# Kernel optimization log

Hardware: AMD Instinct MI355X
Metric: run time of the kernel (lower is better)

The kernel has to match this reference:

```python
import jax, jax.numpy as jnp
import numpy as np

N_NODES = 20000
N_EDGES = 320000
N_QUERY = 100000
D = 256


def _sage_conv(x, adj_row, adj_col, Wl, bl, Wr):
    # PyG SAGEConv with mean aggregation over SparseTensor adj_t:
    #   out = lin_l(mean_{j in N(i)} x_j) + lin_r(x_i)
    # adj_row = destination node, adj_col = source node.
    n = x.shape[0]
    msg = x[adj_col]                                        # [E, D] gather
    agg = jax.ops.segment_sum(msg, adj_row, num_segments=n)  # [N, D]
    deg = jax.ops.segment_sum(jnp.ones((adj_row.shape[0],), x.dtype), adj_row,
                              num_segments=n)
    agg = agg / jnp.maximum(deg, 1.0)[:, None]               # mean reduce
    return agg @ Wl + bl + x @ Wr


def setup_inputs() -> dict:
    key = jax.random.key(0)
    ks = jax.random.split(key, 12)
    s = 1.0 / np.sqrt(D)
    return {
        "adj_row": jax.random.randint(ks[0], (N_EDGES,), 0, N_NODES, dtype=jnp.int32),
        "adj_col": jax.random.randint(ks[1], (N_EDGES,), 0, N_NODES, dtype=jnp.int32),
        "edges": jax.random.randint(ks[2], (2, N_QUERY), 0, N_NODES, dtype=jnp.int32),
        "emb": jax.random.normal(ks[3], (N_NODES, D), jnp.float32),
        "W1l": jax.random.normal(ks[4], (D, D), jnp.float32) * s,
        "b1": jnp.zeros((D,), jnp.float32),
        "W1r": jax.random.normal(ks[5], (D, D), jnp.float32) * s,
        "W2l": jax.random.normal(ks[6], (D, D), jnp.float32) * s,
        "b2": jnp.zeros((D,), jnp.float32),
        "W2r": jax.random.normal(ks[7], (D, D), jnp.float32) * s,
        "Wp1": jax.random.normal(ks[8], (D, D), jnp.float32) * s,
        "bp1": jnp.zeros((D,), jnp.float32),
        "Wp2": jax.random.normal(ks[9], (D, 1), jnp.float32) * s,
        "bp2": jnp.zeros((1,), jnp.float32),
    }


def reference(adj_row, adj_col, edges, emb, W1l, b1, W1r, W2l, b2, W2r,
              Wp1, bp1, Wp2, bp2):
    # SAGE backbone (eval mode: dropout is identity)
    x = _sage_conv(emb, adj_row, adj_col, W1l, b1, W1r)
    x = jax.nn.relu(x)
    x = _sage_conv(x, adj_row, adj_col, W2l, b2, W2r)     # [N, D]
    # LinkPredictor: h = x_i * x_j -> MLP -> sigmoid
    h = x[edges[0]] * x[edges[1]]                          # [Q, D]
    h = jax.nn.relu(h @ Wp1 + bp1)
    return jax.nn.sigmoid(h @ Wp2 + bp2)                   # [Q, 1]
```

## Files before the change

### kernel.cpp

```cpp
#include <hip/hip_runtime.h>
#include <cstddef>

constexpr int NN = 20000;
constexpr int NE = 320000;
constexpr int NQ = 100000;
constexpr int DD = 256;
constexpr int NB = (NN + 255) / 256;

typedef __attribute__((ext_vector_type(8))) short bf16x8;
typedef __attribute__((ext_vector_type(4))) float f32x4;
typedef __attribute__((ext_vector_type(4))) unsigned short u16x4;
typedef __attribute__((ext_vector_type(8))) unsigned short u16x8;

__device__ inline unsigned short f2bf(float f) {
    union { float f; unsigned u; } v; v.f = f;
    unsigned r = v.u + 0x7fffu + ((v.u >> 16) & 1u);
    return (unsigned short)(r >> 16);
}
__device__ inline float bf2f(unsigned short h) {
    union { unsigned u; float f; } t; t.u = ((unsigned)h) << 16;
    return t.f;
}

__global__ __launch_bounds__(256) void k_cast(const float* __restrict__ x,
                                              unsigned short* __restrict__ y,
                                              int* __restrict__ deg) {
    int i = blockIdx.x * 256 + threadIdx.x;
    if (i < NN) deg[i] = 0;
    if (i >= NN * DD / 8) return;
    float4 f0 = *reinterpret_cast<const float4*>(x + (size_t)i * 8);
    float4 f1 = *reinterpret_cast<const float4*>(x + (size_t)i * 8 + 4);
    u16x8 o;
    o[0] = f2bf(f0.x); o[1] = f2bf(f0.y); o[2] = f2bf(f0.z); o[3] = f2bf(f0.w);
    o[4] = f2bf(f1.x); o[5] = f2bf(f1.y); o[6] = f2bf(f1.z); o[7] = f2bf(f1.w);
    *reinterpret_cast<u16x8*>(y + (size_t)i * 8) = o;
}

__global__ __launch_bounds__(256) void k_deg(const int* __restrict__ row,
                                             int* __restrict__ deg) {
    int e = blockIdx.x * 256 + threadIdx.x;
    if (e < NE) atomicAdd(&deg[row[e]], 1);
}

__global__ __launch_bounds__(256) void k_scan1(const int* __restrict__ deg,
                                               int* __restrict__ offs,
                                               int* __restrict__ bsum) {
    __shared__ int wsum[4];
    const int tid = threadIdx.x, lane = tid & 63, wid = tid >> 6;
    int i = blockIdx.x * 256 + tid;
    int v = (i < NN) ? deg[i] : 0;
    int sc = v;
#pragma unroll
    for (int d = 1; d < 64; d <<= 1) {
        int t = __shfl_up(sc, d);
        if (lane >= d) sc += t;
    }
    if (lane == 63) wsum[wid] = sc;
    __syncthreads();
    int wpre = 0;
    for (int w = 0; w < wid; ++w) wpre += wsum[w];
    if (i < NN) offs[i] = wpre + sc - v;
    if (tid == 255) bsum[blockIdx.x] = wpre + sc;
}

__global__ __launch_bounds__(256) void k_scan2(int* __restrict__ bsum) {
    __shared__ int wsum[4];
    const int tid = threadIdx.x, lane = tid & 63, wid = tid >> 6;
    int v = (tid < NB) ? bsum[tid] : 0;
    int sc = v;
#pragma unroll
    for (int d = 1; d < 64; d <<= 1) {
        int t = __shfl_up(sc, d);
        if (lane >= d) sc += t;
    }
    if (lane == 63) wsum[wid] = sc;
    __syncthreads();
    int wpre = 0;
    for (int w = 0; w < wid; ++w) wpre += wsum[w];
    if (tid < NB) bsum[tid] = wpre + sc - v;
}

__global__ __launch_bounds__(256) void k_scan3(const int* __restrict__ deg,
                                               const int* __restrict__ bsum,
                                               int* __restrict__ offs,
                                               int* __restrict__ cursor,
                                               float* __restrict__ recip) {
    int i = blockIdx.x * 256 + threadIdx.x;
    if (i < NN) {
        int o = offs[i] + bsum[i >> 8];
        offs[i] = o;
        cursor[i] = o;
        recip[i] = 1.0f / fmaxf((float)deg[i], 1.0f);
    }
    if (i == 0) offs[NN] = NE;
}

__global__ __launch_bounds__(256) void k_fill(const int* __restrict__ row,
                                              const int* __restrict__ col,
                                              int* __restrict__ cursor,
                                              int* __restrict__ scol) {
    int e = blockIdx.x * 256 + threadIdx.x;
    if (e < NE) {
        int r = row[e];
        int p = atomicAdd(&cursor[r], 1);
        scol[p] = col[e];
    }
}

__global__ __launch_bounds__(256) void k_packs(
    const float* __restrict__ w0, const float* __restrict__ w1,
    const float* __restrict__ w2, const float* __restrict__ w3,
    const float* __restrict__ w4,
    unsigned short* __restrict__ h0, unsigned short* __restrict__ h1,
    unsigned short* __restrict__ h2, unsigned short* __restrict__ h3,
    unsigned short* __restrict__ h4,
    unsigned short* __restrict__ l0, unsigned short* __restrict__ l1,
    unsigned short* __restrict__ l2, unsigned short* __restrict__ l3) {
    int m = blockIdx.x >> 5;
    int idx = (blockIdx.x & 31) * 256 + threadIdx.x;
    const float* W = (m == 0) ? w0 : (m == 1) ? w1 : (m == 2) ? w2 : (m == 3) ? w3 : w4;
    unsigned short* H = (m == 0) ? h0 : (m == 1) ? h1 : (m == 2) ? h2 : (m == 3) ? h3 : h4;
    unsigned short* L = (m == 0) ? l0 : (m == 1) ? l1 : (m == 2) ? l2 : (m == 3) ? l3 : nullptr;
    int t = idx >> 6, lane = idx & 63;
    int kt = t >> 4, nt = t & 15;
    int k0 = kt * 32 + (lane >> 4) * 8;
    int n = nt * 16 + (lane & 15);
    unsigned uh[4], ul[4];
#pragma unroll
    for (int i = 0; i < 4; ++i) {
        float fa = W[(size_t)(k0 + 2 * i) * DD + n];
        float fb = W[(size_t)(k0 + 2 * i + 1) * DD + n];
        unsigned short ha = f2bf(fa), hb = f2bf(fb);
        unsigned short la = f2bf(fa - bf2f(ha)), lb = f2bf(fb - bf2f(hb));
        uh[i] = (unsigned)ha | ((unsigned)hb << 16);
        ul[i] = (unsigned)la | ((unsigned)lb << 16);
    }
    *reinterpret_cast<uint4*>(H + (size_t)idx * 8) = make_uint4(uh[0], uh[1], uh[2], uh[3]);
    if (L)
        *reinterpret_cast<uint4*>(L + (size_t)idx * 8) = make_uint4(ul[0], ul[1], ul[2], ul[3]);
}

__global__ __launch_bounds__(256) void k_lin(
    const unsigned short* __restrict__ A,
    const unsigned short* __restrict__ Wlh, const unsigned short* __restrict__ Wll,
    const unsigned short* __restrict__ Wrh, const unsigned short* __restrict__ Wrl,
    unsigned short* __restrict__ P, unsigned short* __restrict__ Q) {
    const int nq   = blockIdx.x & 3;
    const int mblk = blockIdx.x >> 2;
    const int wave = threadIdx.x >> 6;
    const int lane = threadIdx.x & 63;
    const int row0 = mblk * 64 + wave * 16;
    const int kcol = (lane >> 4) * 8;
    const int ar = min(row0 + (lane & 15), NN - 1);

    f32x4 accP[4], accQ[4];
#pragma unroll
    for (int nt = 0; nt < 4; ++nt) {
        accP[nt] = {0, 0, 0, 0};
        accQ[nt] = {0, 0, 0, 0};
    }

#pragma unroll 2
    for (int kt = 0; kt < 8; ++kt) {
        bf16x8 a1 = *reinterpret_cast<const bf16x8*>(A + (size_t)ar * DD + kt * 32 + kcol);
#pragma unroll
        for (int nt = 0; nt < 4; ++nt) {
            const size_t fo = ((size_t)((kt * 16 + nq * 4 + nt) * 64 + lane)) * 8;
            bf16x8 blh = *reinterpret_cast<const bf16x8*>(Wlh + fo);
            bf16x8 bll = *reinterpret_cast<const bf16x8*>(Wll + fo);
            bf16x8 brh = *reinterpret_cast<const bf16x8*>(Wrh + fo);
            bf16x8 brl = *reinterpret_cast<const bf16x8*>(Wrl + fo);
            accP[nt] = __builtin_amdgcn_mfma_f32_16x16x32_bf16(a1, blh, accP[nt], 0, 0, 0);
            accP[nt] = __builtin_amdgcn_mfma_f32_16x16x32_bf16(a1, bll, accP[nt], 0, 0, 0);
            accQ[nt] = __builtin_amdgcn_mfma_f32_16x16x32_bf16(a1, brh, accQ[nt], 0, 0, 0);
            accQ[nt] = __builtin_amdgcn_mfma_f32_16x16x32_bf16(a1, brl, accQ[nt], 0, 0, 0);
        }
    }

    const int n0 = lane & 15;
    const int rg = (lane >> 4) * 4;
#pragma unroll
    for (int nt = 0; nt < 4; ++nt) {
        int n = (nq * 4 + nt) * 16 + n0;
#pragma unroll
        for (int j = 0; j < 4; ++j) {
            int r = row0 + rg + j;
            if (r < NN) {
                P[(size_t)r * DD + n] = f2bf(accP[nt][j]);
                Q[(size_t)r * DD + n] = f2bf(accQ[nt][j]);
            }
        }
    }
}

template <int RELU>
__global__ __launch_bounds__(256) void k_gath(const int* __restrict__ offs,
                                              const int* __restrict__ scol,
                                              const float* __restrict__ recip,
                                              const unsigned short* __restrict__ P,
                                              const unsigned short* __restrict__ Q,
                                              const float* __restrict__ b,
                                              unsigned short* __restrict__ out) {
    int node = blockIdx.x * 4 + (threadIdx.x >> 6);
    int lane = threadIdx.x & 63;
    if (node >= NN) return;
    int s = offs[node];
    int e = offs[node + 1];
    const int half = lane >> 5;
    const int l32 = lane & 31;
    float acc[8] = {0, 0, 0, 0, 0, 0, 0, 0};
    float acc2[8] = {0, 0, 0, 0, 0, 0, 0, 0};
    int p = s;
    for (; p + 3 < e; p += 4) {
        int c0 = scol[p + half];
        int c1 = scol[p + 2 + half];
        u16x8 v0 = *reinterpret_cast<const u16x8*>(P + (size_t)c0 * DD + l32 * 8);
        u16x8 v1 = *reinterpret_cast<const u16x8*>(P + (size_t)c1 * DD + l32 * 8);
#pragma unroll
        for (int i = 0; i < 8; ++i) {
            acc[i] += bf2f(v0[i]);
            acc2[i] += bf2f(v1[i]);
        }
    }
    for (; p + 1 < e; p += 2) {
        int c0 = scol[p + half];
        u16x8 v0 = *reinterpret_cast<const u16x8*>(P + (size_t)c0 * DD + l32 * 8);
#pragma unroll
        for (int i = 0; i < 8; ++i) acc[i] += bf2f(v0[i]);
    }
    if (p < e && half == 0) {
        int c0 = scol[p];
        u16x8 v0 = *reinterpret_cast<const u16x8*>(P + (size_t)c0 * DD + l32 * 8);
#pragma unroll
        for (int i = 0; i < 8; ++i) acc2[i] += bf2f(v0[i]);
    }
    float rc = recip[node];
    u16x8 q = *reinterpret_cast<const u16x8*>(Q + (size_t)node * DD + l32 * 8);
    float4 b0 = *reinterpret_cast<const float4*>(b + l32 * 8);
    float4 b1 = *reinterpret_cast<const float4*>(b + l32 * 8 + 4);
    float bb[8] = {b0.x, b0.y, b0.z, b0.w, b1.x, b1.y, b1.z, b1.w};
    u16x8 o;
#pragma unroll
    for (int i = 0; i < 8; ++i) {
        float t = acc[i] + acc2[i];
        t += __shfl_xor(t, 32);
        t = t * rc + bf2f(q[i]) + bb[i];
        if (RELU) t = fmaxf(t, 0.0f);
        o[i] = f2bf(t);
    }
    if (half == 0)
        *reinterpret_cast<u16x8*>(out + (size_t)node * DD + l32 * 8) = o;
}

__global__ __launch_bounds__(512, 4) void k_pred(const int* __restrict__ edges,
                                                 const unsigned short* __restrict__ x2,
                                                 const unsigned short* __restrict__ Wp1p,
                                                 const float* __restrict__ bp1,
                                                 const float* __restrict__ Wp2,
                                                 const float* __restrict__ bp2,
                                                 float* __restrict__ out) {
    __shared__ unsigned short sh[128 * 256];
    const int tid = threadIdx.x;
    const int wave = tid >> 6;
    const int lane = tid & 63;
    const int q0 = blockIdx.x * 128;

    const int grow = tid >> 4;
    const int t16 = tid & 15;
#pragma unroll
    for (int s = 0; s < 4; ++s) {
        int r = s * 32 + grow;
        int q = q0 + r;
        u16x8 p0 = {0, 0, 0, 0, 0, 0, 0, 0};
        u16x8 p1 = {0, 0, 0, 0, 0, 0, 0, 0};
        if (q < NQ) {
            int a = edges[q];
            int c = edges[NQ + q];
            const unsigned short* pa = x2 + (size_t)a * DD + t16 * 16;
            const unsigned short* pc = x2 + (size_t)c * DD + t16 * 16;
            u16x8 ua0 = *reinterpret_cast<const u16x8*>(pa);
            u16x8 ua1 = *reinterpret_cast<const u16x8*>(pa + 8);
            u16x8 uc0 = *reinterpret_cast<const u16x8*>(pc);
            u16x8 uc1 = *reinterpret_cast<const u16x8*>(pc + 8);
#pragma unroll
            for (int i = 0; i < 8; ++i) {
                p0[i] = f2bf(bf2f(ua0[i]) * bf2f(uc0[i]));
                p1[i] = f2bf(bf2f(ua1[i]) * bf2f(uc1[i]));
            }
        }
        int swz = (r & 7) << 3;
        *reinterpret_cast<u16x8*>(&sh[r * 256 + ((t16 * 16) ^ swz)]) = p0;
        *reinterpret_cast<u16x8*>(&sh[r * 256 + ((t16 * 16 + 8) ^ swz)]) = p1;
    }
    __syncthreads();

    f32x4 acc[8][2];
#pragma unroll
    for (int m = 0; m < 8; ++m)
#pragma unroll
        for (int n = 0; n < 2; ++n) acc[m][n] = {0, 0, 0, 0};

    const int akoff = (lane >> 4) * 8;
    const int arl = lane & 15;
    for (int kt = 0; kt < 8; ++kt) {
        bf16x8 af[8];
#pragma unroll
        for (int m = 0; m < 8; ++m) {
            int row = m * 16 + arl;
            af[m] = *reinterpret_cast<const bf16x8*>(
                &sh[row * 256 + ((kt * 32 + akoff) ^ ((row & 7) << 3))]);
        }
#pragma unroll
        for (int ntl = 0; ntl < 2; ++ntl) {
            int nt = wave * 2 + ntl;
            bf16x8 bfrag = *reinterpret_cast<const bf16x8*>(
                Wp1p + ((size_t)((kt * 16 + nt) * 64 + lane)) * 8);
#pragma unroll
            for (int m = 0; m < 8; ++m)
                acc[m][ntl] = __builtin_amdgcn_mfma_f32_16x16x32_bf16(af[m], bfrag, acc[m][ntl], 0, 0, 0);
        }
    }

    float rs[8][4];
#pragma unroll
    for (int m = 0; m < 8; ++m)
#pragma unroll
        for (int j = 0; j < 4; ++j) rs[m][j] = 0.0f;
#pragma unroll
    for (int ntl = 0; ntl < 2; ++ntl) {
        int n = (wave * 2 + ntl) * 16 + (lane & 15);
        float bias = bp1[n];
        float w2 = Wp2[n];
#pragma unroll
        for (int m = 0; m < 8; ++m)
#pragma unroll
            for (int j = 0; j < 4; ++j)
                rs[m][j] += fmaxf(acc[m][ntl][j] + bias, 0.0f) * w2;
    }
#pragma unroll
    for (int msk = 1; msk < 16; msk <<= 1) {
#pragma unroll
        for (int m = 0; m < 8; ++m)
#pragma unroll
            for (int j = 0; j < 4; ++j) rs[m][j] += __shfl_xor(rs[m][j], msk);
    }

    float* psum = reinterpret_cast<float*>(sh);
    __syncthreads();
    if ((lane & 15) == 0) {
        int rg = (lane >> 4) * 4;
#pragma unroll
        for (int m = 0; m < 8; ++m)
#pragma unroll
            for (int j = 0; j < 4; ++j)
                psum[wave * 128 + m * 16 + rg + j] = rs[m][j];
    }
    __syncthreads();

    if (tid < 128) {
        int q = q0 + tid;
        if (q < NQ) {
            float z = bp2[0];
#pragma unroll
            for (int w = 0; w < 8; ++w) z += psum[w * 128 + tid];
            out[q] = 1.0f / (1.0f + expf(-z));
        }
    }
}

extern "C" void kernel_launch(void* const* d_in, const int* in_sizes, int n_in,
                              void* d_out, int out_size, void* d_ws, size_t ws_size,
                              hipStream_t stream) {
    const int*   adj_row = (const int*)d_in[0];
    const int*   adj_col = (const int*)d_in[1];
    const int*   edges   = (const int*)d_in[2];
    const float* emb     = (const float*)d_in[3];
    const float* W1l     = (const float*)d_in[4];
    const float* b1      = (const float*)d_in[5];
    const float* W1r     = (const float*)d_in[6];
    const float* W2l     = (const float*)d_in[7];
    const float* b2      = (const float*)d_in[8];
    const float* W2r     = (const float*)d_in[9];
    const float* Wp1     = (const float*)d_in[10];
    const float* bp1     = (const float*)d_in[11];
    const float* Wp2     = (const float*)d_in[12];
    const float* bp2     = (const float*)d_in[13];
    float* out = (float*)d_out;

    const size_t featH = (size_t)NN * DD * 2;
    const size_t packBytes = (size_t)DD * DD * 2;

    char* ws = (char*)d_ws;
    size_t off = 0;
    unsigned short* P  = (unsigned short*)(ws + off); off += featH;
    unsigned short* Q  = (unsigned short*)(ws + off); off += featH;
    unsigned short* x1 = (unsigned short*)(ws + off); off += featH;
    unsigned short* xh = (unsigned short*)(ws + off); off += featH;
    int*   deg    = (int*)(ws + off);   off += (size_t)NN * 4;
    int*   offs   = (int*)(ws + off);   off += (size_t)(NN + 1) * 4;
    int*   cursor = (int*)(ws + off);   off += (size_t)NN * 4;
    float* recip  = (float*)(ws + off); off += (size_t)NN * 4;
    int*   bsum   = (int*)(ws + off);   off += (size_t)NB * 4;
    int*   scol   = (int*)(ws + off);   off += (size_t)NE * 4;
    unsigned short* Wp1p = (unsigned short*)(ws + off); off += packBytes;
    unsigned short* pk[8];
    for (int i = 0; i < 8; ++i) { pk[i] = (unsigned short*)(ws + off); off += packBytes; }

    const int MB4 = ((NN + 63) / 64) * 4;

    k_cast<<<(NN * DD / 8 + 255) / 256, 256, 0, stream>>>(emb, xh, deg);
    k_deg<<<(NE + 255) / 256, 256, 0, stream>>>(adj_row, deg);
    k_scan1<<<NB, 256, 0, stream>>>(deg, offs, bsum);
    k_scan2<<<1, 256, 0, stream>>>(bsum);
    k_scan3<<<NB, 256, 0, stream>>>(deg, bsum, offs, cursor, recip);
    k_fill<<<(NE + 255) / 256, 256, 0, stream>>>(adj_row, adj_col, cursor, scol);
    k_packs<<<160, 256, 0, stream>>>(W1l, W1r, W2l, W2r, Wp1,
                                     pk[0], pk[2], pk[4], pk[6], Wp1p,
                                     pk[1], pk[3], pk[5], pk[7]);

    k_lin<<<MB4, 256, 0, stream>>>(xh, pk[0], pk[1], pk[2], pk[3], P, Q);
    k_gath<1><<<(NN + 3) / 4, 256, 0, stream>>>(offs, scol, recip, P, Q, b1, x1);

    unsigned short* x2 = xh;
    k_lin<<<MB4, 256, 0, stream>>>(x1, pk[4], pk[5], pk[6], pk[7], P, Q);
    k_gath<0><<<(NN + 3) / 4, 256, 0, stream>>>(offs, scol, recip, P, Q, b2, x2);

    k_pred<<<(NQ + 127) / 128, 512, 0, stream>>>(edges, x2, Wp1p, bp1, Wp2, bp2, out);
}
```

Before: 195.4 us.

## Merge cast and weight packing, retile linear GEMM, deepen gather unrolling

Three independent changes. First, the feature cast and the weight pack kernels are merged into one launch to remove one kernel launch. Second, the linear MFMA kernel now gives each wave 32 rows by 32 columns instead of 16 rows by 64 columns, so each B fragment load is reused across two A tiles. Third, the neighbor gather loop processes 8 edges per iteration with 4 independent accumulators to keep more loads in flight. These add register pressure and change the order of the floating-point sums.

```diff
diff --git a/kernel.cpp b/kernel.cpp
--- a/kernel.cpp
+++ b/kernel.cpp
@@ -6,6 +6,7 @@
 constexpr int NQ = 100000;
 constexpr int DD = 256;
 constexpr int NB = (NN + 255) / 256;
+constexpr int CASTB = (NN * DD / 8 + 255) / 256;
 
 typedef __attribute__((ext_vector_type(8))) short bf16x8;
 typedef __attribute__((ext_vector_type(4))) float f32x4;
@@ -22,18 +23,53 @@
     return t.f;
 }
 
-__global__ __launch_bounds__(256) void k_cast(const float* __restrict__ x,
-                                              unsigned short* __restrict__ y,
-                                              int* __restrict__ deg) {
-    int i = blockIdx.x * 256 + threadIdx.x;
-    if (i < NN) deg[i] = 0;
-    if (i >= NN * DD / 8) return;
-    float4 f0 = *reinterpret_cast<const float4*>(x + (size_t)i * 8);
-    float4 f1 = *reinterpret_cast<const float4*>(x + (size_t)i * 8 + 4);
-    u16x8 o;
-    o[0] = f2bf(f0.x); o[1] = f2bf(f0.y); o[2] = f2bf(f0.z); o[3] = f2bf(f0.w);
-    o[4] = f2bf(f1.x); o[5] = f2bf(f1.y); o[6] = f2bf(f1.z); o[7] = f2bf(f1.w);
-    *reinterpret_cast<u16x8*>(y + (size_t)i * 8) = o;
+__global__ __launch_bounds__(256) void k_castpack(
+    const float* __restrict__ x, unsigned short* __restrict__ y,
+    int* __restrict__ deg,
+    const float* __restrict__ w0, const float* __restrict__ w1,
+    const float* __restrict__ w2, const float* __restrict__ w3,
+    const float* __restrict__ w4,
+    unsigned short* __restrict__ h0, unsigned short* __restrict__ h1,
+    unsigned short* __restrict__ h2, unsigned short* __restrict__ h3,
+    unsigned short* __restrict__ h4,
+    unsigned short* __restrict__ l0, unsigned short* __restrict__ l1,
+    unsigned short* __restrict__ l2, unsigned short* __restrict__ l3) {
+    const int bid = blockIdx.x;
+    if (bid < CASTB) {
+        int i = bid * 256 + threadIdx.x;
+        if (i < NN) deg[i] = 0;
+        if (i >= NN * DD / 8) return;
+        float4 f0 = *reinterpret_cast<const float4*>(x + (size_t)i * 8);
+        float4 f1 = *reinterpret_cast<const float4*>(x + (size_t)i * 8 + 4);
+        u16x8 o;
+        o[0] = f2bf(f0.x); o[1] = f2bf(f0.y); o[2] = f2bf(f0.z); o[3] = f2bf(f0.w);
+        o[4] = f2bf(f1.x); o[5] = f2bf(f1.y); o[6] = f2bf(f1.z); o[7] = f2bf(f1.w);
+        *reinterpret_cast<u16x8*>(y + (size_t)i * 8) = o;
+        return;
+    }
+    int mb = bid - CASTB;
+    int m = mb >> 5;
+    int idx = (mb & 31) * 256 + threadIdx.x;
+    const float* W = (m == 0) ? w0 : (m == 1) ? w1 : (m == 2) ? w2 : (m == 3) ? w3 : w4;
+    unsigned short* H = (m == 0) ? h0 : (m == 1) ? h1 : (m == 2) ? h2 : (m == 3) ? h3 : h4;
+    unsigned short* L = (m == 0) ? l0 : (m == 1) ? l1 : (m == 2) ? l2 : (m == 3) ? l3 : nullptr;
+    int t = idx >> 6, lane = idx & 63;
+    int kt = t >> 4, nt = t & 15;
+    int k0 = kt * 32 + (lane >> 4) * 8;
+    int n = nt * 16 + (lane & 15);
+    unsigned uh[4], ul[4];
+#pragma unroll
+    for (int i = 0; i < 4; ++i) {
+        float fa = W[(size_t)(k0 + 2 * i) * DD + n];
+        float fb = W[(size_t)(k0 + 2 * i + 1) * DD + n];
+        unsigned short ha = f2bf(fa), hb = f2bf(fb);
+        unsigned short la = f2bf(fa - bf2f(ha)), lb = f2bf(fb - bf2f(hb));
+        uh[i] = (unsigned)ha | ((unsigned)hb << 16);
+        ul[i] = (unsigned)la | ((unsigned)lb << 16);
+    }
+    *reinterpret_cast<uint4*>(H + (size_t)idx * 8) = make_uint4(uh[0], uh[1], uh[2], uh[3]);
+    if (L)
+        *reinterpret_cast<uint4*>(L + (size_t)idx * 8) = make_uint4(ul[0], ul[1], ul[2], ul[3]);
 }
 
 __global__ __launch_bounds__(256) void k_deg(const int* __restrict__ row,
@@ -107,90 +143,67 @@
     }
 }
 
-__global__ __launch_bounds__(256) void k_packs(
-    const float* __restrict__ w0, const float* __restrict__ w1,
-    const float* __restrict__ w2, const float* __restrict__ w3,
-    const float* __restrict__ w4,
-    unsigned short* __restrict__ h0, unsigned short* __restrict__ h1,
-    unsigned short* __restrict__ h2, unsigned short* __restrict__ h3,
-    unsigned short* __restrict__ h4,
-    unsigned short* __restrict__ l0, unsigned short* __restrict__ l1,
-    unsigned short* __restrict__ l2, unsigned short* __restrict__ l3) {
-    int m = blockIdx.x >> 5;
-    int idx = (blockIdx.x & 31) * 256 + threadIdx.x;
-    const float* W = (m == 0) ? w0 : (m == 1) ? w1 : (m == 2) ? w2 : (m == 3) ? w3 : w4;
-    unsigned short* H = (m == 0) ? h0 : (m == 1) ? h1 : (m == 2) ? h2 : (m == 3) ? h3 : h4;
-    unsigned short* L = (m == 0) ? l0 : (m == 1) ? l1 : (m == 2) ? l2 : (m == 3) ? l3 : nullptr;
-    int t = idx >> 6, lane = idx & 63;
-    int kt = t >> 4, nt = t & 15;
-    int k0 = kt * 32 + (lane >> 4) * 8;
-    int n = nt * 16 + (lane & 15);
-    unsigned uh[4], ul[4];
-#pragma unroll
-    for (int i = 0; i < 4; ++i) {
-        float fa = W[(size_t)(k0 + 2 * i) * DD + n];
-        float fb = W[(size_t)(k0 + 2 * i + 1) * DD + n];
-        unsigned short ha = f2bf(fa), hb = f2bf(fb);
-        unsigned short la = f2bf(fa - bf2f(ha)), lb = f2bf(fb - bf2f(hb));
-        uh[i] = (unsigned)ha | ((unsigned)hb << 16);
-        ul[i] = (unsigned)la | ((unsigned)lb << 16);
-    }
-    *reinterpret_cast<uint4*>(H + (size_t)idx * 8) = make_uint4(uh[0], uh[1], uh[2], uh[3]);
-    if (L)
-        *reinterpret_cast<uint4*>(L + (size_t)idx * 8) = make_uint4(ul[0], ul[1], ul[2], ul[3]);
-}
-
 __global__ __launch_bounds__(256) void k_lin(
     const unsigned short* __restrict__ A,
     const unsigned short* __restrict__ Wlh, const unsigned short* __restrict__ Wll,
     const unsigned short* __restrict__ Wrh, const unsigned short* __restrict__ Wrl,
     unsigned short* __restrict__ P, unsigned short* __restrict__ Q) {
-    const int nq   = blockIdx.x & 3;
-    const int mblk = blockIdx.x >> 2;
+    const int ns   = blockIdx.x & 7;
+    const int mblk = blockIdx.x >> 3;
     const int wave = threadIdx.x >> 6;
     const int lane = threadIdx.x & 63;
-    const int row0 = mblk * 64 + wave * 16;
+    const int row0 = mblk * 128 + wave * 32;
     const int kcol = (lane >> 4) * 8;
-    const int ar = min(row0 + (lane & 15), NN - 1);
-
-    f32x4 accP[4], accQ[4];
-#pragma unroll
-    for (int nt = 0; nt < 4; ++nt) {
-        accP[nt] = {0, 0, 0, 0};
-        accQ[nt] = {0, 0, 0, 0};
-    }
+    const int ar0 = min(row0 + (lane & 15), NN - 1);
+    const int ar1 = min(row0 + 16 + (lane & 15), NN - 1);
+
+    f32x4 accP[2][2], accQ[2][2];
+#pragma unroll
+    for (int mt = 0; mt < 2; ++mt)
+#pragma unroll
+        for (int nt = 0; nt < 2; ++nt) {
+            accP[mt][nt] = {0, 0, 0, 0};
+            accQ[mt][nt] = {0, 0, 0, 0};
+        }
 
 #pragma unroll 2
     for (int kt = 0; kt < 8; ++kt) {
-        bf16x8 a1 = *reinterpret_cast<const bf16x8*>(A + (size_t)ar * DD + kt * 32 + kcol);
-#pragma unroll
-        for (int nt = 0; nt < 4; ++nt) {
-            const size_t fo = ((size_t)((kt * 16 + nq * 4 + nt) * 64 + lane)) * 8;
+        bf16x8 a0 = *reinterpret_cast<const bf16x8*>(A + (size_t)ar0 * DD + kt * 32 + kcol);
+        bf16x8 a1 = *reinterpret_cast<const bf16x8*>(A + (size_t)ar1 * DD + kt * 32 + kcol);
+#pragma unroll
+        for (int nt = 0; nt < 2; ++nt) {
+            const size_t fo = ((size_t)((kt * 16 + ns * 2 + nt) * 64 + lane)) * 8;
             bf16x8 blh = *reinterpret_cast<const bf16x8*>(Wlh + fo);
             bf16x8 bll = *reinterpret_cast<const bf16x8*>(Wll + fo);
             bf16x8 brh = *reinterpret_cast<const bf16x8*>(Wrh + fo);
             bf16x8 brl = *reinterpret_cast<const bf16x8*>(Wrl + fo);
-            accP[nt] = __builtin_amdgcn_mfma_f32_16x16x32_bf16(a1, blh, accP[nt], 0, 0, 0);
-            accP[nt] = __builtin_amdgcn_mfma_f32_16x16x32_bf16(a1, bll, accP[nt], 0, 0, 0);
-            accQ[nt] = __builtin_amdgcn_mfma_f32_16x16x32_bf16(a1, brh, accQ[nt], 0, 0, 0);
-            accQ[nt] = __builtin_amdgcn_mfma_f32_16x16x32_bf16(a1, brl, accQ[nt], 0, 0, 0);
+            accP[0][nt] = __builtin_amdgcn_mfma_f32_16x16x32_bf16(a0, blh, accP[0][nt], 0, 0, 0);
+            accP[1][nt] = __builtin_amdgcn_mfma_f32_16x16x32_bf16(a1, blh, accP[1][nt], 0, 0, 0);
+            accP[0][nt] = __builtin_amdgcn_mfma_f32_16x16x32_bf16(a0, bll, accP[0][nt], 0, 0, 0);
+            accP[1][nt] = __builtin_amdgcn_mfma_f32_16x16x32_bf16(a1, bll, accP[1][nt], 0, 0, 0);
+            accQ[0][nt] = __builtin_amdgcn_mfma_f32_16x16x32_bf16(a0, brh, accQ[0][nt], 0, 0, 0);
+            accQ[1][nt] = __builtin_amdgcn_mfma_f32_16x16x32_bf16(a1, brh, accQ[1][nt], 0, 0, 0);
+            accQ[0][nt] = __builtin_amdgcn_mfma_f32_16x16x32_bf16(a0, brl, accQ[0][nt], 0, 0, 0);
+            accQ[1][nt] = __builtin_amdgcn_mfma_f32_16x16x32_bf16(a1, brl, accQ[1][nt], 0, 0, 0);
         }
     }
 
     const int n0 = lane & 15;
     const int rg = (lane >> 4) * 4;
 #pragma unroll
-    for (int nt = 0; nt < 4; ++nt) {
-        int n = (nq * 4 + nt) * 16 + n0;
-#pragma unroll
-        for (int j = 0; j < 4; ++j) {
-            int r = row0 + rg + j;
-            if (r < NN) {
-                P[(size_t)r * DD + n] = f2bf(accP[nt][j]);
-                Q[(size_t)r * DD + n] = f2bf(accQ[nt][j]);
+    for (int mt = 0; mt < 2; ++mt)
+#pragma unroll
+        for (int nt = 0; nt < 2; ++nt) {
+            int n = (ns * 2 + nt) * 16 + n0;
+#pragma unroll
+            for (int j = 0; j < 4; ++j) {
+                int r = row0 + mt * 16 + rg + j;
+                if (r < NN) {
+                    P[(size_t)r * DD + n] = f2bf(accP[mt][nt][j]);
+                    Q[(size_t)r * DD + n] = f2bf(accQ[mt][nt][j]);
+                }
             }
         }
-    }
 }
 
 template <int RELU>
@@ -208,31 +221,33 @@
     int e = offs[node + 1];
     const int half = lane >> 5;
     const int l32 = lane & 31;
-    float acc[8] = {0, 0, 0, 0, 0, 0, 0, 0};
-    float acc2[8] = {0, 0, 0, 0, 0, 0, 0, 0};
+    float a0[8] = {0,0,0,0,0,0,0,0}, a1[8] = {0,0,0,0,0,0,0,0};
+    float a2[8] = {0,0,0,0,0,0,0,0}, a3[8] = {0,0,0,0,0,0,0,0};
     int p = s;
-    for (; p + 3 < e; p += 4) {
-        int c0 = scol[p + half];
-        int c1 = scol[p + 2 + half];
+    for (; p + 7 < e; p += 8) {
+        int base = p + 4 * half;
+        int c0 = scol[base], c1 = scol[base + 1], c2 = scol[base + 2], c3 = scol[base + 3];
         u16x8 v0 = *reinterpret_cast<const u16x8*>(P + (size_t)c0 * DD + l32 * 8);
         u16x8 v1 = *reinterpret_cast<const u16x8*>(P + (size_t)c1 * DD + l32 * 8);
+        u16x8 v2 = *reinterpret_cast<const u16x8*>(P + (size_t)c2 * DD + l32 * 8);
+        u16x8 v3 = *reinterpret_cast<const u16x8*>(P + (size_t)c3 * DD + l32 * 8);
 #pragma unroll
         for (int i = 0; i < 8; ++i) {
-            acc[i] += bf2f(v0[i]);
-            acc2[i] += bf2f(v1[i]);
+            a0[i] += bf2f(v0[i]); a1[i] += bf2f(v1[i]);
+            a2[i] += bf2f(v2[i]); a3[i] += bf2f(v3[i]);
         }
     }
     for (; p + 1 < e; p += 2) {
         int c0 = scol[p + half];
         u16x8 v0 = *reinterpret_cast<const u16x8*>(P + (size_t)c0 * DD + l32 * 8);
 #pragma unroll
-        for (int i = 0; i < 8; ++i) acc[i] += bf2f(v0[i]);
+        for (int i = 0; i < 8; ++i) a0[i] += bf2f(v0[i]);
     }
     if (p < e && half == 0) {
         int c0 = scol[p];
         u16x8 v0 = *reinterpret_cast<const u16x8*>(P + (size_t)c0 * DD + l32 * 8);
 #pragma unroll
-        for (int i = 0; i < 8; ++i) acc2[i] += bf2f(v0[i]);
+        for (int i = 0; i < 8; ++i) a1[i] += bf2f(v0[i]);
     }
     float rc = recip[node];
     u16x8 q = *reinterpret_cast<const u16x8*>(Q + (size_t)node * DD + l32 * 8);
@@ -242,7 +257,7 @@
     u16x8 o;
 #pragma unroll
     for (int i = 0; i < 8; ++i) {
-        float t = acc[i] + acc2[i];
+        float t = a0[i] + a1[i] + a2[i] + a3[i];
         t += __shfl_xor(t, 32);
         t = t * rc + bf2f(q[i]) + bb[i];
         if (RELU) t = fmaxf(t, 0.0f);
@@ -406,23 +421,23 @@
     unsigned short* pk[8];
     for (int i = 0; i < 8; ++i) { pk[i] = (unsigned short*)(ws + off); off += packBytes; }
 
-    const int MB4 = ((NN + 63) / 64) * 4;
-
-    k_cast<<<(NN * DD / 8 + 255) / 256, 256, 0, stream>>>(emb, xh, deg);
+    const int MB8 = ((NN + 127) / 128) * 8;
+
+    k_castpack<<<CASTB + 160, 256, 0, stream>>>(emb, xh, deg,
+                                                W1l, W1r, W2l, W2r, Wp1,
+                                                pk[0], pk[2], pk[4], pk[6], Wp1p,
+                                                pk[1], pk[3], pk[5], pk[7]);
     k_deg<<<(NE + 255) / 256, 256, 0, stream>>>(adj_row, deg);
     k_scan1<<<NB, 256, 0, stream>>>(deg, offs, bsum);
     k_scan2<<<1, 256, 0, stream>>>(bsum);
     k_scan3<<<NB, 256, 0, stream>>>(deg, bsum, offs, cursor, recip);
     k_fill<<<(NE + 255) / 256, 256, 0, stream>>>(adj_row, adj_col, cursor, scol);
-    k_packs<<<160, 256, 0, stream>>>(W1l, W1r, W2l, W2r, Wp1,
-                                     pk[0], pk[2], pk[4], pk[6], Wp1p,
-                                     pk[1], pk[3], pk[5], pk[7]);
-
-    k_lin<<<MB4, 256, 0, stream>>>(xh, pk[0], pk[1], pk[2], pk[3], P, Q);
+
+    k_lin<<<MB8, 256, 0, stream>>>(xh, pk[0], pk[1], pk[2], pk[3], P, Q);
     k_gath<1><<<(NN + 3) / 4, 256, 0, stream>>>(offs, scol, recip, P, Q, b1, x1);
 
     unsigned short* x2 = xh;
-    k_lin<<<MB4, 256, 0, stream>>>(x1, pk[4], pk[5], pk[6], pk[7], P, Q);
+    k_lin<<<MB8, 256, 0, stream>>>(x1, pk[4], pk[5], pk[6], pk[7], P, Q);
     k_gath<0><<<(NN + 3) / 4, 256, 0, stream>>>(offs, scol, recip, P, Q, b2, x2);
 
     k_pred<<<(NQ + 127) / 128, 512, 0, stream>>>(edges, x2, Wp1p, bp1, Wp2, bp2, out);
```

Measured after the change: 198.0 us. No clear change (+1.3%).
